# Optimization experiments

Hardware: AMD Instinct MI355X
Metric: run time of the kernel (lower is better)

The kernel has to match this reference:

```python
import jax, jax.numpy as jnp
import numpy as np

EPS = 1e-06
K = 10
N, M, D, C = 65536, 1024, 2, 3


def setup_inputs() -> dict:
    key = jax.random.key(0)
    k1, k2, k3, k4 = jax.random.split(key, 4)
    x = jax.random.uniform(k1, (N, D), dtype=jnp.float32)            # query points (pixels)
    mus = jax.random.uniform(k2, (1, M, D), dtype=jnp.float32)        # gaussian means
    A = 0.1 * jax.random.normal(k3, (1, M, D, D), dtype=jnp.float32)  # random factor
    covs = A @ jnp.swapaxes(A, -1, -2) + 0.01 * jnp.eye(D, dtype=jnp.float32)  # SPD covariances
    cols = jax.random.uniform(k4, (1, M, C), dtype=jnp.float32)       # per-gaussian RGB
    return {"x": x, "mus": mus, "covs": covs, "cols": cols}


def reference(x, mus, covs, cols):
    # d: [N, M, D] point-to-mean offsets
    d = x[:, None, :] - mus[0]
    # solve covs @ s = d for each (point, gaussian) pair -> [N, M, D]
    s = jnp.linalg.solve(covs[0], d[..., None])[..., 0]
    # quadratic form d^T Sigma^{-1} d -> gaussian weights [N, M]
    gauss = jnp.exp(-0.5 * jnp.einsum('nmd,nmd->nm', d, s))
    k = min(K, mus.shape[1])
    vals, idx = jax.lax.top_k(gauss, k)              # [N, k]
    top_cols = cols[0][idx]                           # [N, k, C]
    raw = jnp.einsum('nk,nkc->nc', vals, top_cols)    # weighted color sum
    return raw / (vals.sum(-1, keepdims=True) + EPS)  # normalized [N, C]
```

## Files before the change

kernel.cpp:

```cpp
#include <hip/hip_runtime.h>
#include <stdint.h>

#define MG 1024
#define KTOP 10
#define EPSF 1e-6f
#define CXc 24
#define CYc 16
#define NCELL (CXc * CYc)
#define SCX 96
#define SCY 32
#define NSUB (SCX * SCY)
#define CAPS 40
#define OVCAP 256
#define RHO 0.03757f
#define CSTRIDE 1040
#define CPAD 16
#define POISON 0xAAAAAAAAu

typedef unsigned long long u64;
typedef unsigned short u16;

__global__ __launch_bounds__(256) void k_prep(
    const float* __restrict__ x, const float* __restrict__ mus,
    const float* __restrict__ covs,
    uint32_t* __restrict__ counts, uint32_t* __restrict__ ovc,
    u16* __restrict__ ovlist, u16* __restrict__ buckets,
    float4* __restrict__ grec, float* __restrict__ grecC,
    u16* __restrict__ candM, uint32_t* __restrict__ ncand, int N)
{
    const int t = threadIdx.x, blk = blockIdx.x;
    if (blk < 256) {
        const int n = blk * 256 + t;
        if (n < MG) {
            const float4 cv = ((const float4*)covs)[n];
            const float2 mu = ((const float2*)mus)[n];
            const float inv = 1.0f / (cv.x * cv.w - cv.y * cv.z);
            grec[n]  = make_float4(mu.x, mu.y, -0.5f * cv.w * inv, cv.y * inv);
            grecC[n] = -0.5f * cv.x * inv;
        }
        if (n >= N) return;
        const float2 xv = ((const float2*)x)[n];
        int six = (int)(xv.x * SCX); six = six < 0 ? 0 : (six > SCX - 1 ? SCX - 1 : six);
        int siy = (int)(xv.y * SCY); siy = siy < 0 ? 0 : (siy > SCY - 1 ? SCY - 1 : siy);
        const int sub = siy * SCX + six;
        const uint32_t r = atomicAdd(&counts[sub * CPAD], 1u) - POISON;
        if (r < CAPS) buckets[sub * CAPS + r] = (u16)n;
        else { const uint32_t o = atomicAdd(ovc, 1u) - POISON; if (o < OVCAP) ovlist[o] = (u16)n; }
        return;
    }
    const int lane = t & 63;
    const int c = (blk - 256) * 4 + (t >> 6);
    const float cx = ((float)(c % CXc) + 0.5f) / (float)CXc;
    const float cy = ((float)(c / CXc) + 0.5f) / (float)CYc;
    const float INF = __builtin_huge_valf();

    float D10[KTOP], Uv[16];
    #pragma unroll
    for (int i = 0; i < KTOP; ++i) D10[i] = -INF;

    #pragma unroll
    for (int j = 0; j < 16; ++j) {
        const int m = j * 64 + lane;
        const float4 cv = ((const float4*)covs)[m];
        const float2 mu = ((const float2*)mus)[m];
        const float inv = 1.0f / (cv.x * cv.w - cv.y * cv.z);
        const float A = -0.5f * cv.w * inv, B = cv.y * inv, Cc = -0.5f * cv.x * inv;
        const float dx = cx - mu.x, dy = cy - mu.y;
        const float qc = fmaf(fmaf(A, dx, B * dy), dx, Cc * (dy * dy));
        const float S00 = -2.0f * A, S01 = -B, S11 = -2.0f * Cc;
        const float sx = S00 * dx + S01 * dy, sy = S01 * dx + S11 * dy;
        const float slack = sqrtf(fmaf(sx, sx, sy * sy)) * RHO;
        const float lr2 = 0.5f * (S00 + S11) * (RHO * RHO);
        const float eps = 1e-3f * (1.0f + fabsf(qc) + slack);
        Uv[j] = qc + slack + eps;
        const float D = qc - slack - lr2 - eps;
        bool cg[KTOP];
        #pragma unroll
        for (int i = 0; i < KTOP; ++i) cg[i] = D10[i] >= D;
        #pragma unroll
        for (int i = KTOP - 1; i >= 1; --i)
            D10[i] = cg[i] ? D10[i] : (cg[i - 1] ? D : D10[i - 1]);
        D10[0] = cg[0] ? D10[0] : D;
    }
    #pragma unroll
    for (int s = 1; s < 64; s <<= 1) {
        float ob[KTOP], na[KTOP];
        #pragma unroll
        for (int i = 0; i < KTOP; ++i) ob[i] = __shfl_xor(D10[i], s);
        #pragma unroll
        for (int i = 0; i < KTOP; ++i) {
            float best = -INF;
            #pragma unroll
            for (int j = 0; j <= i + 1 && j <= KTOP; ++j) {
                const int l = i + 1 - j;
                if (l > KTOP) continue;
                const float av = (j == 0) ? INF : D10[j - 1];
                const float bv = (l == 0) ? INF : ob[l - 1];
                best = fmaxf(best, fminf(av, bv));
            }
            na[i] = best;
        }
        #pragma unroll
        for (int i = 0; i < KTOP; ++i) D10[i] = na[i];
    }
    const float L = D10[KTOP - 1];

    const int base = c * CSTRIDE;
    const u64 below = (lane == 0) ? 0ull : ((~0ull) >> (64 - lane));
    int total = 0;
    #pragma unroll
    for (int j = 0; j < 16; ++j) {
        const bool keep = (Uv[j] >= L);
        const u64 bal = __ballot(keep);
        if (keep) {
            const int slot = total + (int)__popcll(bal & below);
            candM[base + slot] = (u16)(j * 64 + lane);
        }
        total += (int)__popcll(bal);
    }
    if (lane == 0) ncand[c] = (uint32_t)total;
}

__global__ __launch_bounds__(128) void k_main(
    const float* __restrict__ x, const float* __restrict__ cols,
    const float4* __restrict__ grec, const float* __restrict__ grecC,
    const uint32_t* __restrict__ counts, const uint32_t* __restrict__ ovc,
    const u16* __restrict__ ovlist, const u16* __restrict__ buckets,
    const u16* __restrict__ candM, const uint32_t* __restrict__ ncand,
    float* __restrict__ out, int N)
{
    __shared__ float4 l4[CSTRIDE];
    __shared__ __align__(16) float lC[CSTRIDE];
    __shared__ __align__(16) uint32_t lM[CSTRIDE];

    const int t = threadIdx.x;
    const int lane = t & 63, wv = t >> 6;
    const int b = blockIdx.x;

    u64 topk[KTOP];
    const u64 SENT = ((u64)0x007FFFFFull) << 10;
    #pragma unroll
    for (int j = 0; j < KTOP; ++j) topk[j] = SENT;
    float thr = __uint_as_float(0xff800000u);

    auto net_insert = [&](u64 key) {
        bool cg[KTOP];
        #pragma unroll
        for (int j = 0; j < KTOP; ++j) cg[j] = topk[j] >= key;
        #pragma unroll
        for (int j = KTOP - 1; j >= 1; --j)
            topk[j] = cg[j] ? topk[j] : (cg[j - 1] ? key : topk[j - 1]);
        topk[0] = cg[0] ? topk[0] : key;
    };
    auto ins = [&](float q, int m) {
        if (__any(q >= thr)) {
            const uint32_t bb = __float_as_uint(q);
            const uint32_t msk = (uint32_t)((int32_t)bb >> 31) | 0x80000000u;
            net_insert(((u64)(bb ^ msk) << 10) | (u64)(MG - 1 - m));
            const uint32_t kb = (uint32_t)(topk[KTOP - 1] >> 10);
            const uint32_t db = ((int32_t)kb < 0) ? (kb ^ 0x80000000u) : ~kb;
            thr = __uint_as_float(db);
        }
    };

    int pp = 0; bool valid = false;

    if (b >= 3 * NCELL) {
        const uint32_t oc = min(ovc[0] - POISON, (uint32_t)OVCAP);
        const uint32_t gi = (uint32_t)((b - 3 * NCELL) * 128 + t);
        if (__ballot(gi < oc) == 0ull) return;
        int p = -1;
        if (gi < oc) p = (int)ovlist[gi];
        valid = (p >= 0);
        const int p0lane = __shfl(p, 0);
        pp = valid ? p : (p0lane >= 0 ? p0lane : 0);
        const float2 xv = ((const float2*)x)[pp];
        const float x0 = xv.x, x1 = xv.y;
        for (int m = 0; m < MG; m += 4) {
            const float4 g0 = grec[m], g1 = grec[m + 1], g2 = grec[m + 2], g3 = grec[m + 3];
            const float4 c4 = *(const float4*)&grecC[m];
            const float dx0 = x0 - g0.x, dy0 = x1 - g0.y;
            const float dx1 = x0 - g1.x, dy1 = x1 - g1.y;
            const float dx2 = x0 - g2.x, dy2 = x1 - g2.y;
            const float dx3 = x0 - g3.x, dy3 = x1 - g3.y;
            const float q0 = fmaf(fmaf(g0.z, dx0, g0.w * dy0), dx0, c4.x * (dy0 * dy0));
            const float q1 = fmaf(fmaf(g1.z, dx1, g1.w * dy1), dx1, c4.y * (dy1 * dy1));
            const float q2 = fmaf(fmaf(g2.z, dx2, g2.w * dy2), dx2, c4.z * (dy2 * dy2));
            const float q3 = fmaf(fmaf(g3.z, dx3, g3.w * dy3), dx3, c4.w * (dy3 * dy3));
            const float qm = fmaxf(fmaxf(q0, q1), fmaxf(q2, q3));
            if (__any(qm >= thr)) {
                ins(q0, m); ins(q1, m + 1); ins(q2, m + 2); ins(q3, m + 3);
            }
        }
    } else {
        const int c = b / 3, h = b % 3;
        const int ccx = c % CXc, ccy = c / CXc;
        int pre[9]; pre[0] = 0;
        int subs[8];
        #pragma unroll
        for (int j = 0; j < 8; ++j) {
            const int six = 4 * ccx + (j & 3), siy = 2 * ccy + (j >> 2);
            subs[j] = siy * SCX + six;
            const uint32_t cj = counts[subs[j] * CPAD] - POISON;
            pre[j + 1] = pre[j] + (int)min(cj, (uint32_t)CAPS);
        }
        const int cnt = pre[8];
        if (h * 128 >= cnt) return;

        const int nc = (int)min(ncand[c], (uint32_t)(CSTRIDE - 4));
        const int ntot = (nc + 3) & ~3;
        const int cbase = c * CSTRIDE;
        for (int i = t; i < ntot; i += 128) {
            if (i < nc) {
                const int m = (int)candM[cbase + i];
                l4[i] = grec[m];
                lC[i] = grecC[m];
                lM[i] = (uint32_t)m;
            } else {
                l4[i] = make_float4(3e30f, 3e30f, -1.0f, 0.0f);
                lC[i] = -1.0f;
                lM[i] = 0u;
            }
        }
        __syncthreads();

        const int slot = (h * 2 + wv) * 64 + lane;
        if ((h * 2 + wv) * 64 >= cnt) return;
        int p = -1;
        if (slot < cnt) {
            int j = 0;
            #pragma unroll
            for (int k = 1; k < 8; ++k) j += (slot >= pre[k]) ? 1 : 0;
            p = (int)buckets[subs[j] * CAPS + (slot - pre[j])];
        }
        valid = (p >= 0);
        const int p0lane = __shfl(p, 0);
        pp = valid ? p : p0lane;
        const float2 xv = ((const float2*)x)[pp];
        const float x0 = xv.x, x1 = xv.y;

        for (int i2 = 0; i2 < ntot; i2 += 4) {
            const float4 g0 = l4[i2], g1 = l4[i2 + 1], g2 = l4[i2 + 2], g3 = l4[i2 + 3];
            const float4 c4 = *(const float4*)&lC[i2];
            const uint4  m4 = *(const uint4*)&lM[i2];
            const float dx0 = x0 - g0.x, dy0 = x1 - g0.y;
            const float dx1 = x0 - g1.x, dy1 = x1 - g1.y;
            const float dx2 = x0 - g2.x, dy2 = x1 - g2.y;
            const float dx3 = x0 - g3.x, dy3 = x1 - g3.y;
            const float q0 = fmaf(fmaf(g0.z, dx0, g0.w * dy0), dx0, c4.x * (dy0 * dy0));
            const float q1 = fmaf(fmaf(g1.z, dx1, g1.w * dy1), dx1, c4.y * (dy1 * dy1));
            const float q2 = fmaf(fmaf(g2.z, dx2, g2.w * dy2), dx2, c4.z * (dy2 * dy2));
            const float q3 = fmaf(fmaf(g3.z, dx3, g3.w * dy3), dx3, c4.w * (dy3 * dy3));
            const float qm = fmaxf(fmaxf(q0, q1), fmaxf(q2, q3));
            if (__any(qm >= thr)) {
                ins(q0, (int)m4.x); ins(q1, (int)m4.y);
                ins(q2, (int)m4.z); ins(q3, (int)m4.w);
            }
        }
    }

    float vsum = 0.0f, rc = 0.0f, gc = 0.0f, bc = 0.0f;
    #pragma unroll
    for (int j = 0; j < KTOP; ++j) {
        const u64 key = topk[j];
        const int m = (MG - 1) - (int)(key & 1023u);
        const uint32_t kb = (uint32_t)(key >> 10);
        const uint32_t bb = ((int32_t)kb < 0) ? (kb ^ 0x80000000u) : ~kb;
        const float v = __expf(__uint_as_float(bb));
        vsum += v;
        rc = fmaf(v, cols[3 * m + 0], rc);
        gc = fmaf(v, cols[3 * m + 1], gc);
        bc = fmaf(v, cols[3 * m + 2], bc);
    }
    const float s = 1.0f / (vsum + EPSF);
    if (valid) {
        out[pp * 3 + 0] = rc * s;
        out[pp * 3 + 1] = gc * s;
        out[pp * 3 + 2] = bc * s;
    }
}

extern "C" void kernel_launch(void* const* d_in, const int* in_sizes, int n_in,
                              void* d_out, int out_size, void* d_ws, size_t ws_size,
                              hipStream_t stream) {
    const float* x    = (const float*)d_in[0];
    const float* mus  = (const float*)d_in[1];
    const float* covs = (const float*)d_in[2];
    const float* cols = (const float*)d_in[3];
    float* out = (float*)d_out;
    const int N = in_sizes[0] / 2;

    uint32_t* counts = (uint32_t*)d_ws;
    uint32_t* ovc    = counts + NSUB * CPAD;
    u16*      ovlist = (u16*)(ovc + 16);
    uintptr_t a = (uintptr_t)(ovlist + OVCAP);
    a = (a + 15) & ~(uintptr_t)15;
    float4*   grec   = (float4*)a;
    float*    grecC  = (float*)(grec + MG);
    u16*      buckets= (u16*)(grecC + MG);
    uint32_t* ncand  = (uint32_t*)(buckets + NSUB * CAPS);
    u16*      candM  = (u16*)(ncand + NCELL);
    const size_t need = ((char*)(candM + NCELL * CSTRIDE)) - (char*)d_ws;

    if (ws_size >= need) {
        k_prep<<<256 + NCELL / 4, 256, 0, stream>>>(x, mus, covs, counts, ovc,
                                                    ovlist, buckets, grec, grecC,
                                                    candM, ncand, N);
        k_main<<<3 * NCELL + 2, 128, 0, stream>>>(x, cols, grec, grecC,
                                                  counts, ovc, ovlist, buckets,
                                                  candM, ncand, out, N);
    }
}
```

Before: 91.70 us.

## Shrink spatial cells to two subcells with smaller candidate radius and staging

Doubles the cell grid resolution in each dimension so each block covers two subcells (up to 128 points) instead of eight, and halves the candidate radius so each cell's gaussian candidate list is shorter. Shared-memory staging is capped at a smaller size, which frees LDS and should raise occupancy. Cells whose candidate list exceeds the cap fall back to a full scan of all gaussians from global memory. The risk is that the smaller radius misses true top-k gaussians, or that the fallback path is hit often. The launch now uses one block per cell instead of three blocks per cell.

```diff
diff --git a/kernel.cpp b/kernel.cpp
--- a/kernel.cpp
+++ b/kernel.cpp
@@ -4,16 +4,17 @@
 #define MG 1024
 #define KTOP 10
 #define EPSF 1e-6f
-#define CXc 24
-#define CYc 16
+#define CXc 48
+#define CYc 32
 #define NCELL (CXc * CYc)
 #define SCX 96
 #define SCY 32
 #define NSUB (SCX * SCY)
-#define CAPS 40
+#define CAPS 64
 #define OVCAP 256
-#define RHO 0.03757f
+#define RHO 0.01878f
 #define CSTRIDE 1040
+#define MAXC 508
 #define CPAD 16
 #define POISON 0xAAAAAAAAu
 
@@ -129,9 +130,9 @@
     const u16* __restrict__ candM, const uint32_t* __restrict__ ncand,
     float* __restrict__ out, int N)
 {
-    __shared__ float4 l4[CSTRIDE];
-    __shared__ __align__(16) float lC[CSTRIDE];
-    __shared__ __align__(16) uint32_t lM[CSTRIDE];
+    __shared__ float4 l4[MAXC + 4];
+    __shared__ __align__(16) float lC[MAXC + 4];
+    __shared__ __align__(16) uint32_t lM[MAXC + 4];
 
     const int t = threadIdx.x;
     const int lane = t & 63, wv = t >> 6;
@@ -162,20 +163,7 @@
             thr = __uint_as_float(db);
         }
     };
-
-    int pp = 0; bool valid = false;
-
-    if (b >= 3 * NCELL) {
-        const uint32_t oc = min(ovc[0] - POISON, (uint32_t)OVCAP);
-        const uint32_t gi = (uint32_t)((b - 3 * NCELL) * 128 + t);
-        if (__ballot(gi < oc) == 0ull) return;
-        int p = -1;
-        if (gi < oc) p = (int)ovlist[gi];
-        valid = (p >= 0);
-        const int p0lane = __shfl(p, 0);
-        pp = valid ? p : (p0lane >= 0 ? p0lane : 0);
-        const float2 xv = ((const float2*)x)[pp];
-        const float x0 = xv.x, x1 = xv.y;
+    auto full_scan = [&](float x0, float x1) {
         for (int m = 0; m < MG; m += 4) {
             const float4 g0 = grec[m], g1 = grec[m + 1], g2 = grec[m + 2], g3 = grec[m + 3];
             const float4 c4 = *(const float4*)&grecC[m];
@@ -192,46 +180,56 @@
                 ins(q0, m); ins(q1, m + 1); ins(q2, m + 2); ins(q3, m + 3);
             }
         }
+    };
+
+    int pp = 0; bool valid = false;
+
+    if (b >= NCELL) {
+        const uint32_t oc = min(ovc[0] - POISON, (uint32_t)OVCAP);
+        const uint32_t gi = (uint32_t)((b - NCELL) * 128 + t);
+        if (__ballot(gi < oc) == 0ull) return;
+        int p = -1;
+        if (gi < oc) p = (int)ovlist[gi];
+        valid = (p >= 0);
+        const int p0lane = __shfl(p, 0);
+        pp = valid ? p : (p0lane >= 0 ? p0lane : 0);
+        const float2 xv = ((const float2*)x)[pp];
+        full_scan(xv.x, xv.y);
     } else {
-        const int c = b / 3, h = b % 3;
+        const int c = b;
         const int ccx = c % CXc, ccy = c / CXc;
-        int pre[9]; pre[0] = 0;
-        int subs[8];
-        #pragma unroll
-        for (int j = 0; j < 8; ++j) {
-            const int six = 4 * ccx + (j & 3), siy = 2 * ccy + (j >> 2);
-            subs[j] = siy * SCX + six;
-            const uint32_t cj = counts[subs[j] * CPAD] - POISON;
-            pre[j + 1] = pre[j] + (int)min(cj, (uint32_t)CAPS);
-        }
-        const int cnt = pre[8];
-        if (h * 128 >= cnt) return;
+        const int sub0 = ccy * SCX + 2 * ccx;
+        const int cnt0 = (int)min(counts[sub0 * CPAD] - POISON, (uint32_t)CAPS);
+        const int cnt1 = (int)min(counts[(sub0 + 1) * CPAD] - POISON, (uint32_t)CAPS);
+        const int cnt = cnt0 + cnt1;
+        if (cnt == 0) return;
 
         const int nc = (int)min(ncand[c], (uint32_t)(CSTRIDE - 4));
-        const int ntot = (nc + 3) & ~3;
-        const int cbase = c * CSTRIDE;
-        for (int i = t; i < ntot; i += 128) {
-            if (i < nc) {
-                const int m = (int)candM[cbase + i];
-                l4[i] = grec[m];
-                lC[i] = grecC[m];
-                lM[i] = (uint32_t)m;
-            } else {
-                l4[i] = make_float4(3e30f, 3e30f, -1.0f, 0.0f);
-                lC[i] = -1.0f;
-                lM[i] = 0u;
+        const bool staged = (nc <= MAXC);
+        if (staged) {
+            const int ntot = (nc + 3) & ~3;
+            const int cbase = c * CSTRIDE;
+            for (int i = t; i < ntot; i += 128) {
+                if (i < nc) {
+                    const int m = (int)candM[cbase + i];
+                    l4[i] = grec[m];
+                    lC[i] = grecC[m];
+                    lM[i] = (uint32_t)m;
+                } else {
+                    l4[i] = make_float4(3e30f, 3e30f, -1.0f, 0.0f);
+                    lC[i] = -1.0f;
+                    lM[i] = 0u;
+                }
             }
-        }
-        __syncthreads();
-
-        const int slot = (h * 2 + wv) * 64 + lane;
-        if ((h * 2 + wv) * 64 >= cnt) return;
+            __syncthreads();
+        }
+
+        const int slot = wv * 64 + lane;
+        if (wv * 64 >= cnt) return;
         int p = -1;
         if (slot < cnt) {
-            int j = 0;
-            #pragma unroll
-            for (int k = 1; k < 8; ++k) j += (slot >= pre[k]) ? 1 : 0;
-            p = (int)buckets[subs[j] * CAPS + (slot - pre[j])];
+            p = (slot < cnt0) ? (int)buckets[sub0 * CAPS + slot]
+                              : (int)buckets[(sub0 + 1) * CAPS + (slot - cnt0)];
         }
         valid = (p >= 0);
         const int p0lane = __shfl(p, 0);
@@ -239,23 +237,28 @@
         const float2 xv = ((const float2*)x)[pp];
         const float x0 = xv.x, x1 = xv.y;
 
-        for (int i2 = 0; i2 < ntot; i2 += 4) {
-            const float4 g0 = l4[i2], g1 = l4[i2 + 1], g2 = l4[i2 + 2], g3 = l4[i2 + 3];
-            const float4 c4 = *(const float4*)&lC[i2];
-            const uint4  m4 = *(const uint4*)&lM[i2];
-            const float dx0 = x0 - g0.x, dy0 = x1 - g0.y;
-            const float dx1 = x0 - g1.x, dy1 = x1 - g1.y;
-            const float dx2 = x0 - g2.x, dy2 = x1 - g2.y;
-            const float dx3 = x0 - g3.x, dy3 = x1 - g3.y;
-            const float q0 = fmaf(fmaf(g0.z, dx0, g0.w * dy0), dx0, c4.x * (dy0 * dy0));
-            const float q1 = fmaf(fmaf(g1.z, dx1, g1.w * dy1), dx1, c4.y * (dy1 * dy1));
-            const float q2 = fmaf(fmaf(g2.z, dx2, g2.w * dy2), dx2, c4.z * (dy2 * dy2));
-            const float q3 = fmaf(fmaf(g3.z, dx3, g3.w * dy3), dx3, c4.w * (dy3 * dy3));
-            const float qm = fmaxf(fmaxf(q0, q1), fmaxf(q2, q3));
-            if (__any(qm >= thr)) {
-                ins(q0, (int)m4.x); ins(q1, (int)m4.y);
-                ins(q2, (int)m4.z); ins(q3, (int)m4.w);
+        if (staged) {
+            const int ntot = (nc + 3) & ~3;
+            for (int i2 = 0; i2 < ntot; i2 += 4) {
+                const float4 g0 = l4[i2], g1 = l4[i2+1], g2 = l4[i2+2], g3 = l4[i2+3];
+                const float4 c4 = *(const float4*)&lC[i2];
+                const uint4  m4 = *(const uint4*)&lM[i2];
+                const float dx0 = x0 - g0.x, dy0 = x1 - g0.y;
+                const float dx1 = x0 - g1.x, dy1 = x1 - g1.y;
+                const float dx2 = x0 - g2.x, dy2 = x1 - g2.y;
+                const float dx3 = x0 - g3.x, dy3 = x1 - g3.y;
+                const float q0 = fmaf(fmaf(g0.z, dx0, g0.w * dy0), dx0, c4.x * (dy0 * dy0));
+                const float q1 = fmaf(fmaf(g1.z, dx1, g1.w * dy1), dx1, c4.y * (dy1 * dy1));
+                const float q2 = fmaf(fmaf(g2.z, dx2, g2.w * dy2), dx2, c4.z * (dy2 * dy2));
+                const float q3 = fmaf(fmaf(g3.z, dx3, g3.w * dy3), dx3, c4.w * (dy3 * dy3));
+                const float qm = fmaxf(fmaxf(q0, q1), fmaxf(q2, q3));
+                if (__any(qm >= thr)) {
+                    ins(q0, (int)m4.x); ins(q1, (int)m4.y);
+                    ins(q2, (int)m4.z); ins(q3, (int)m4.w);
+                }
             }
+        } else {
+            full_scan(x0, x1);
         }
     }
 
@@ -306,8 +309,8 @@
         k_prep<<<256 + NCELL / 4, 256, 0, stream>>>(x, mus, covs, counts, ovc,
                                                     ovlist, buckets, grec, grecC,
                                                     candM, ncand, N);
-        k_main<<<3 * NCELL + 2, 128, 0, stream>>>(x, cols, grec, grecC,
-                                                  counts, ovc, ovlist, buckets,
-                                                  candM, ncand, out, N);
+        k_main<<<NCELL + 2, 128, 0, stream>>>(x, cols, grec, grecC,
+                                              counts, ovc, ovlist, buckets,
+                                              candM, ncand, out, N);
     }
 }
```

After: 86.76 us. 5.4% less time.
